# Kernel optimization log

Hardware: AMD Instinct MI355X
Metric: run time of the kernel (lower is better)

Reference implementation:

```python
import jax, jax.numpy as jnp
import numpy as np

D_MODEL = 1024
NHEAD = 8
HEAD_DIM = D_MODEL // NHEAD
D_FF = 4096
EPS_ATTN = 1e-6
EPS_LN = 1e-5


def _layernorm(x, g, b):
    mu = jnp.mean(x, axis=-1, keepdims=True)
    var = jnp.var(x, axis=-1, keepdims=True)
    return (x - mu) * jax.lax.rsqrt(var + EPS_LN) * g + b


def _linear_attention(q, k, v):
    # q,k,v: [N, L, H, D]
    Q = jax.nn.elu(q) + 1.0
    K = jax.nn.elu(k) + 1.0
    v_length = v.shape[1]
    v = v / v_length
    KV = jnp.einsum('nshd,nshv->nhdv', K, v)           # [N,H,D,D]
    Z = 1.0 / (jnp.einsum('nlhd,nhd->nlh', Q, K.sum(axis=1)) + EPS_ATTN)
    out = jnp.einsum('nlhd,nhdv,nlh->nlhv', Q, KV, Z) * v_length
    return out


def setup_inputs() -> dict:
    key = jax.random.key(0)
    ks = jax.random.split(key, 12)
    s = 1.0 / np.sqrt(D_MODEL)
    sf = 1.0 / np.sqrt(D_FF)
    return {
        'x': jax.random.normal(ks[0], (2, 4096, D_MODEL), jnp.float32),
        'wq': jax.random.normal(ks[1], (D_MODEL, D_MODEL), jnp.float32) * s,
        'wk': jax.random.normal(ks[2], (D_MODEL, D_MODEL), jnp.float32) * s,
        'wv': jax.random.normal(ks[3], (D_MODEL, D_MODEL), jnp.float32) * s,
        'w1': jax.random.normal(ks[4], (D_FF, D_MODEL), jnp.float32) * s,
        'b1': jnp.zeros((D_FF,), jnp.float32),
        'w2': jax.random.normal(ks[5], (D_MODEL, D_FF), jnp.float32) * sf,
        'b2': jnp.zeros((D_MODEL,), jnp.float32),
        'g1': jnp.ones((D_MODEL,), jnp.float32),
        'be1': jnp.zeros((D_MODEL,), jnp.float32),
        'g2': jnp.ones((D_MODEL,), jnp.float32),
        'be2': jnp.zeros((D_MODEL,), jnp.float32),
    }


def reference(x, wq, wk, wv, w1, b1, w2, b2, g1, be1, g2, be2):
    N, L, C = x.shape
    # pre-norm self attention
    x2 = _layernorm(x, g1, be1)
    q = (x2 @ wq.T).reshape(N, L, NHEAD, HEAD_DIM)
    k = (x2 @ wk.T).reshape(N, L, NHEAD, HEAD_DIM)
    v = (x2 @ wv.T).reshape(N, L, NHEAD, HEAD_DIM)
    msg = _linear_attention(q, k, v).reshape(N, L, C)
    x = x + msg
    # MLP block
    x2 = _layernorm(x, g2, be2)
    h = jax.nn.gelu(x2 @ w1.T + b1, approximate=False)
    x = x + (h @ w2.T + b2)
    return x
```

## Files before the change

kernel.cpp:

```cpp
#include <hip/hip_runtime.h>
#include <hip/hip_bf16.h>
#include <math.h>

typedef __bf16 bf16x8 __attribute__((ext_vector_type(8)));
typedef __bf16 bf16x4 __attribute__((ext_vector_type(4)));
typedef float f32x4 __attribute__((ext_vector_type(4)));

#define DEVI __device__ __forceinline__

DEVI void gload_lds16(const __bf16* g, __bf16* l) {
    __builtin_amdgcn_global_load_lds(
        (const __attribute__((address_space(1))) unsigned int*)g,
        (__attribute__((address_space(3))) unsigned int*)l, 16, 0, 0);
}

DEVI float fast_erf(float x) {
    const float ax = __builtin_fabsf(x);
    const float t = __builtin_amdgcn_rcpf(__builtin_fmaf(0.3275911f, ax, 1.0f));
    float p = __builtin_fmaf(1.061405429f, t, -1.453152027f);
    p = __builtin_fmaf(p, t, 1.421413741f);
    p = __builtin_fmaf(p, t, -0.284496736f);
    p = __builtin_fmaf(p, t, 0.254829592f);
    const float e = __expf(-ax * ax);
    const float r = __builtin_fmaf(-p * t, e, 1.0f);
    return __builtin_copysignf(r, x);
}

DEVI float gelu_exact(float v) {
    return 0.5f * v * (1.0f + fast_erf(v * 0.70710678118654752f));
}

DEVI int swz128(int row, int col) { return row * 128 + (col ^ ((row & 7) << 3)); }

__global__ void sniff_kernel(const unsigned short* __restrict__ x, int* flags) {
    const int tid = threadIdx.x;
    const unsigned short u = x[tid * 2];
    const int e = (u >> 7) & 0xFF;
    const int zero = (u == 0) ? 1 : 0;
    const int sane = ((e >= 0x71 && e <= 0x8E) || ((u & 0x7FFF) == 0)) ? 1 : 0;
    const unsigned long long mz = __ballot(zero != 0);
    const unsigned long long ms = __ballot(sane != 0);
    __shared__ int wz[4], wsn[4];
    if ((tid & 63) == 0) { wz[tid >> 6] = __popcll(mz); wsn[tid >> 6] = __popcll(ms); }
    __syncthreads();
    if (tid == 0) {
        const int nz = wz[0] + wz[1] + wz[2] + wz[3];
        const int ns = wsn[0] + wsn[1] + wsn[2] + wsn[3];
        flags[0] = (nz >= 192 || ns < 128) ? 1 : 0;
    }
}

DEVI void conv8(const void* src, __bf16* dst, int si, int di, int isf32) {
    if (isf32) {
        const float* s = (const float*)src + si;
        bf16x8 o;
#pragma unroll
        for (int j = 0; j < 8; j++) o[j] = (__bf16)s[j];
        *(bf16x8*)(dst + di) = o;
    } else {
        *(uint4*)(dst + di) = *(const uint4*)((const __bf16*)src + si);
    }
}

__global__ __launch_bounds__(256) void convert_kernel(const void* __restrict__ src,
                                                      __bf16* __restrict__ dst, int n,
                                                      const int* __restrict__ flags) {
    const int i = (blockIdx.x * 256 + threadIdx.x) * 8;
    if (i >= n) return;
    conv8(src, dst, i, i, flags[0]);
}

__global__ __launch_bounds__(256) void convert3_kernel(const void* s0, const void* s1,
                                                       const void* s2, __bf16* __restrict__ dst,
                                                       const int* __restrict__ flags) {
    const int i = (blockIdx.x * 256 + threadIdx.x) * 8;
    const int which = i >> 20;
    const int off = i & 1048575;
    const void* s = (which == 0) ? s0 : ((which == 1) ? s1 : s2);
    conv8(s, dst, off, i, flags[0]);
}

struct Ptr6 { const void* p[6]; };
__global__ __launch_bounds__(256) void convert_small(Ptr6 srcs, __bf16* __restrict__ d0,
                                                     __bf16* __restrict__ d1,
                                                     const int* __restrict__ flags) {
    const int idx = (blockIdx.x * 256 + threadIdx.x) * 8;
    if (idx >= 9216) return;
    const int f = flags[0];
    if (idx < 4096) {
        conv8(srcs.p[0], d0, idx, idx, f);
    } else {
        const int j = idx - 4096;
        conv8(srcs.p[1 + (j >> 10)], d1, j & 1023, j, f);
    }
}

__global__ __launch_bounds__(256) void convert_ln_kernel(
    const void* __restrict__ src, const __bf16* __restrict__ g,
    const __bf16* __restrict__ b, __bf16* __restrict__ cx,
    __bf16* __restrict__ x2, const int* __restrict__ flags) {
    const size_t row = blockIdx.x;
    const int tid = threadIdx.x;
    float v[4];
    if (flags[0]) {
        const float4 f = *((const float4*)((const float*)src + row * 1024) + tid);
        v[0] = f.x; v[1] = f.y; v[2] = f.z; v[3] = f.w;
    } else {
        const bf16x4 f = *((const bf16x4*)((const __bf16*)src + row * 1024) + tid);
#pragma unroll
        for (int i = 0; i < 4; i++) v[i] = (float)f[i];
    }
    bf16x4 o;
#pragma unroll
    for (int i = 0; i < 4; i++) o[i] = (__bf16)v[i];
    *((bf16x4*)(cx + row * 1024) + tid) = o;

    float s = v[0] + v[1] + v[2] + v[3];
    float s2 = v[0] * v[0] + v[1] * v[1] + v[2] * v[2] + v[3] * v[3];
#pragma unroll
    for (int m = 32; m >= 1; m >>= 1) {
        s += __shfl_xor(s, m, 64);
        s2 += __shfl_xor(s2, m, 64);
    }
    __shared__ float rs[4], rs2[4];
    const int wave = tid >> 6, lane = tid & 63;
    if (lane == 0) { rs[wave] = s; rs2[wave] = s2; }
    __syncthreads();
    s = rs[0] + rs[1] + rs[2] + rs[3];
    s2 = rs2[0] + rs2[1] + rs2[2] + rs2[3];
    const float mu = s * (1.0f / 1024.0f);
    const float var = s2 * (1.0f / 1024.0f) - mu * mu;
    const float inv = rsqrtf(var + 1e-5f);
#pragma unroll
    for (int i = 0; i < 4; i++) {
        const int c = tid * 4 + i;
        x2[row * 1024 + c] = (__bf16)((v[i] - mu) * inv * (float)g[c] + (float)b[c]);
    }
}

template <typename T>
__global__ __launch_bounds__(256) void ln_kernel(const T* __restrict__ x,
                                                 const __bf16* __restrict__ g,
                                                 const __bf16* __restrict__ b,
                                                 __bf16* __restrict__ out) {
    const size_t row = blockIdx.x;
    const T* xr = x + row * 1024;
    const int tid = threadIdx.x;
    float v[4];
#pragma unroll
    for (int i = 0; i < 4; i++) v[i] = (float)xr[tid * 4 + i];
    float s = v[0] + v[1] + v[2] + v[3];
    float s2 = v[0] * v[0] + v[1] * v[1] + v[2] * v[2] + v[3] * v[3];
#pragma unroll
    for (int m = 32; m >= 1; m >>= 1) {
        s += __shfl_xor(s, m, 64);
        s2 += __shfl_xor(s2, m, 64);
    }
    __shared__ float rs[4], rs2[4];
    const int wave = tid >> 6, lane = tid & 63;
    if (lane == 0) { rs[wave] = s; rs2[wave] = s2; }
    __syncthreads();
    s = rs[0] + rs[1] + rs[2] + rs[3];
    s2 = rs2[0] + rs2[1] + rs2[2] + rs2[3];
    const float mu = s * (1.0f / 1024.0f);
    const float var = s2 * (1.0f / 1024.0f) - mu * mu;
    const float inv = rsqrtf(var + 1e-5f);
#pragma unroll
    for (int i = 0; i < 4; i++) {
        const int c = tid * 4 + i;
        out[row * 1024 + c] = (__bf16)((v[i] - mu) * inv * (float)g[c] + (float)b[c]);
    }
}

enum { EP_NONE = 0, EP_ELU1 = 1, EP_BIAS_GELU = 2, EP_BIAS_RES = 3, EP_QKV = 4 };

template <int EP, typename OutT>
__global__ __launch_bounds__(256, 4) void gemm_bt(
    const __bf16* __restrict__ A, const __bf16* __restrict__ B,
    const __bf16* __restrict__ bias, const float* resid,
    OutT* C, int M, int N, int K) {
    const int nwg = gridDim.x * gridDim.y;
    int bid = blockIdx.y * gridDim.x + blockIdx.x;
    bid = (bid & 7) * (nwg >> 3) + (bid >> 3);
    const int bm = bid / gridDim.x, bn = bid % gridDim.x;

    const int tid = threadIdx.x;
    const int wave = tid >> 6, lane = tid & 63;
    const int wm = wave & 1, wn = wave >> 1;
    const int lm = lane & 15, lq = lane >> 4;

    __shared__ __align__(16) __bf16 Asmem[2][128 * 32];
    __shared__ __align__(16) __bf16 Bsmem[2][128 * 32];

    f32x4 acc[4][4] = {};

    const __bf16* Abase = A + (size_t)bm * 128 * K;
    const __bf16* Bbase = B + (size_t)bn * 128 * K;

    const int sr = tid >> 2;
    const int sc = (((tid & 3) ^ ((tid >> 3) & 3))) << 3;
    const int wb = wave * 512;

    const __bf16* Ap0 = Abase + (size_t)sr * K + sc;
    const __bf16* Ap1 = Abase + (size_t)(sr + 64) * K + sc;
    const __bf16* Bp0 = Bbase + (size_t)sr * K + sc;
    const __bf16* Bp1 = Bbase + (size_t)(sr + 64) * K + sc;

    const int rg = ((lq ^ ((lm >> 1) & 3))) << 3;

#define STAGE(b, kk)                              \
    do {                                          \
        gload_lds16(Ap0 + (kk), &Asmem[b][wb]);   \
        gload_lds16(Ap1 + (kk), &Asmem[b][2048 + wb]); \
        gload_lds16(Bp0 + (kk), &Bsmem[b][wb]);   \
        gload_lds16(Bp1 + (kk), &Bsmem[b][2048 + wb]); \
    } while (0)

    STAGE(0, 0);
    __syncthreads();
    int cur = 0;
    for (int k0 = 0; k0 < K; k0 += 32) {
        if (k0 + 32 < K) STAGE(cur ^ 1, k0 + 32);
        bf16x8 af[4], bfv[4];
#pragma unroll
        for (int i = 0; i < 4; i++) {
            af[i]  = *(const bf16x8*)&Asmem[cur][(wm * 64 + i * 16 + lm) * 32 + rg];
            bfv[i] = *(const bf16x8*)&Bsmem[cur][(wn * 64 + i * 16 + lm) * 32 + rg];
        }
#pragma unroll
        for (int i = 0; i < 4; i++)
#pragma unroll
            for (int j = 0; j < 4; j++)
                acc[i][j] = __builtin_amdgcn_mfma_f32_16x16x32_bf16(af[i], bfv[j], acc[i][j], 0, 0, 0);
        __syncthreads();
        cur ^= 1;
    }
#undef STAGE

    const int row0 = bm * 128 + wm * 64;
    const int col0 = bn * 128 + wn * 64;
#pragma unroll
    for (int i = 0; i < 4; i++) {
#pragma unroll
        for (int j = 0; j < 4; j++) {
            const int col = col0 + j * 16 + lm;
#pragma unroll
            for (int r = 0; r < 4; r++) {
                const int row = row0 + i * 16 + lq * 4 + r;
                float v = acc[i][j][r];
                if (EP == EP_QKV) {
                    const int which = col >> 10;
                    if (which < 2) v = (v > 0.0f) ? (v + 1.0f) : __expf(v);
                    ((__bf16*)C)[(size_t)which * 8388608 + (size_t)row * 1024 + (col & 1023)] = (__bf16)v;
                    continue;
                }
                if (EP == EP_ELU1) {
                    v = (v > 0.0f) ? (v + 1.0f) : __expf(v);
                } else if (EP == EP_BIAS_GELU) {
                    v += (float)bias[col];
                    v = gelu_exact(v);
                } else if (EP == EP_BIAS_RES) {
                    v += (float)bias[col];
                    v += resid[(size_t)row * N + col];
                }
                C[(size_t)row * N + col] = (OutT)v;
            }
        }
    }
}

__global__ __launch_bounds__(512, 2) void gemm256_gelu(
    const __bf16* __restrict__ A, const __bf16* __restrict__ B,
    const __bf16* __restrict__ bias, __bf16* __restrict__ C,
    int M, int N, int K) {
    const int nwg = gridDim.x * gridDim.y;
    int bid = blockIdx.y * gridDim.x + blockIdx.x;
    bid = (bid & 7) * (nwg >> 3) + (bid >> 3);
    const int bm = bid / gridDim.x, bn = bid % gridDim.x;

    const int tid = threadIdx.x;
    const int wave = tid >> 6, lane = tid & 63;
    const int wm = wave >> 2, wn = wave & 3;
    const int lm = lane & 15, lq = lane >> 4;

    __shared__ __align__(16) __bf16 Asmem[2][256 * 64];
    __shared__ __align__(16) __bf16 Bsmem[2][256 * 64];

    f32x4 acc[8][4] = {};

    const int sr = tid >> 3;
    const int sc = (((tid & 7) ^ ((tid >> 3) & 7))) << 3;
    const int wdst = wave * 512;

    const __bf16* Ap[4];
    const __bf16* Bp[4];
#pragma unroll
    for (int p = 0; p < 4; p++) {
        Ap[p] = A + (size_t)(bm * 256 + p * 64 + sr) * K + sc;
        Bp[p] = B + (size_t)(bn * 256 + p * 64 + sr) * K + sc;
    }

#define STAGE256(b, kk)                                          \
    do {                                                         \
        _Pragma("unroll")                                        \
        for (int p = 0; p < 4; p++) {                            \
            gload_lds16(Ap[p] + (kk), &Asmem[b][p * 4096 + wdst]); \
            gload_lds16(Bp[p] + (kk), &Bsmem[b][p * 4096 + wdst]); \
        }                                                        \
    } while (0)

    STAGE256(0, 0);
    STAGE256(1, 64);
    asm volatile("s_waitcnt vmcnt(8)" ::: "memory");
    __builtin_amdgcn_s_barrier();
    asm volatile("" ::: "memory");

    const int gsw = lm & 7;
    const int nt = K >> 6;
    int cur = 0;
    for (int t = 0; t < nt; ++t) {
#pragma unroll
        for (int ks = 0; ks < 2; ks++) {
            const int rg = ((ks * 4 + lq) ^ gsw) << 3;
            bf16x8 af[8], bv[4];
#pragma unroll
            for (int i = 0; i < 8; i++)
                af[i] = *(const bf16x8*)&Asmem[cur][(wm * 128 + i * 16 + lm) * 64 + rg];
#pragma unroll
            for (int j = 0; j < 4; j++)
                bv[j] = *(const bf16x8*)&Bsmem[cur][(wn * 64 + j * 16 + lm) * 64 + rg];
            __builtin_amdgcn_s_setprio(1);
#pragma unroll
            for (int i = 0; i < 8; i++)
#pragma unroll
                for (int j = 0; j < 4; j++)
                    acc[i][j] = __builtin_amdgcn_mfma_f32_16x16x32_bf16(af[i], bv[j], acc[i][j], 0, 0, 0);
            __builtin_amdgcn_s_setprio(0);
        }
        asm volatile("" ::: "memory");
        __builtin_amdgcn_s_barrier();
        asm volatile("" ::: "memory");
        if (t + 2 < nt) {
            STAGE256(cur, (t + 2) << 6);
            asm volatile("s_waitcnt vmcnt(8)" ::: "memory");
        } else {
            asm volatile("s_waitcnt vmcnt(0)" ::: "memory");
        }
        __builtin_amdgcn_s_barrier();
        asm volatile("" ::: "memory");
        cur ^= 1;
    }
#undef STAGE256

    const int row0 = bm * 256 + wm * 128;
    const int col0 = bn * 256 + wn * 64;
#pragma unroll
    for (int i = 0; i < 8; i++) {
#pragma unroll
        for (int j = 0; j < 4; j++) {
            const int col = col0 + j * 16 + lm;
            const float bcol = (float)bias[col];
#pragma unroll
            for (int r = 0; r < 4; r++) {
                const int row = row0 + i * 16 + lq * 4 + r;
                C[(size_t)row * N + col] = (__bf16)gelu_exact(acc[i][j][r] + bcol);
            }
        }
    }
}

__global__ __launch_bounds__(256, 2) void gemm_bt_k64(
    const __bf16* __restrict__ A, const __bf16* __restrict__ B,
    const __bf16* __restrict__ bias, const float* resid,
    float* C, int M, int N, int K) {
    const int nwg = gridDim.x * gridDim.y;
    int bid = blockIdx.y * gridDim.x + blockIdx.x;
    bid = (bid & 7) * (nwg >> 3) + (bid >> 3);
    const int bm = bid / gridDim.x, bn = bid % gridDim.x;

    const int tid = threadIdx.x;
    const int wave = tid >> 6, lane = tid & 63;
    const int wm = wave & 1, wn = wave >> 1;
    const int lm = lane & 15, lq = lane >> 4;

    __shared__ __align__(16) __bf16 Asmem[2][128 * 64];
    __shared__ __align__(16) __bf16 Bsmem[2][128 * 64];

    f32x4 acc[4][4] = {};

    const __bf16* Abase = A + (size_t)bm * 128 * K;
    const __bf16* Bbase = B + (size_t)bn * 128 * K;

    const int sr = tid >> 3;
    const int sc = (((tid & 7) ^ ((tid >> 3) & 7))) << 3;
    const int wb = wave * 512;

    const __bf16* Ap[4];
    const __bf16* Bp[4];
#pragma unroll
    for (int p = 0; p < 4; p++) {
        Ap[p] = Abase + (size_t)(p * 32 + sr) * K + sc;
        Bp[p] = Bbase + (size_t)(p * 32 + sr) * K + sc;
    }

#define STAGE64(b, kk)                                        \
    do {                                                      \
        _Pragma("unroll")                                     \
        for (int p = 0; p < 4; p++) {                         \
            gload_lds16(Ap[p] + (kk), &Asmem[b][p * 2048 + wb]); \
            gload_lds16(Bp[p] + (kk), &Bsmem[b][p * 2048 + wb]); \
        }                                                     \
    } while (0)

    STAGE64(0, 0);
    __syncthreads();
    int cur = 0;
    for (int k0 = 0; k0 < K; k0 += 64) {
        if (k0 + 64 < K) STAGE64(cur ^ 1, k0 + 64);
        bf16x8 af[2][4], bfv[2][4];
#pragma unroll
        for (int h = 0; h < 2; h++) {
            const int rg = ((h * 4 + lq) ^ (lm & 7)) << 3;
#pragma unroll
            for (int i = 0; i < 4; i++) {
                af[h][i]  = *(const bf16x8*)&Asmem[cur][(wm * 64 + i * 16 + lm) * 64 + rg];
                bfv[h][i] = *(const bf16x8*)&Bsmem[cur][(wn * 64 + i * 16 + lm) * 64 + rg];
            }
        }
#pragma unroll
        for (int h = 0; h < 2; h++)
#pragma unroll
            for (int i = 0; i < 4; i++)
#pragma unroll
                for (int j = 0; j < 4; j++)
                    acc[i][j] = __builtin_amdgcn_mfma_f32_16x16x32_bf16(af[h][i], bfv[h][j], acc[i][j], 0, 0, 0);
        __syncthreads();
        cur ^= 1;
    }
#undef STAGE64

    const int row0 = bm * 128 + wm * 64;
    const int col0 = bn * 128 + wn * 64;
#pragma unroll
    for (int i = 0; i < 4; i++) {
#pragma unroll
        for (int j = 0; j < 4; j++) {
            const int col = col0 + j * 16 + lm;
            const float bcol = (float)bias[col];
#pragma unroll
            for (int r = 0; r < 4; r++) {
                const int row = row0 + i * 16 + lq * 4 + r;
                float v = acc[i][j][r] + bcol;
                v += resid[(size_t)row * N + col];
                C[(size_t)row * N + col] = v;
            }
        }
    }
}

__global__ __launch_bounds__(256) void kv_kernel(const __bf16* __restrict__ Kf,
                                                 const __bf16* __restrict__ Vf,
                                                 float* __restrict__ pkv,
                                                 float* __restrict__ pks) {
    const int nh = blockIdx.x, sc = blockIdx.y, vh = blockIdx.z;
    const int n = nh >> 3, h = nh & 7;
    const int tid = threadIdx.x;
    const int tv = tid & 15, td = tid >> 4;
    __shared__ __align__(16) __bf16 Kt[32 * 128];
    __shared__ __align__(16) __bf16 Vt[32 * 64];
    float acc[8][4] = {};
    float ks[8] = {};
    const size_t rowbase = (size_t)n * 4096 + (size_t)sc * 256;
    for (int s0 = 0; s0 < 256; s0 += 32) {
#pragma unroll
        for (int rep = 0; rep < 2; rep++) {
            const int s = tid + rep * 256;
            const int r = s >> 4, cs = (s & 15) * 8;
            const size_t gidx = (rowbase + s0 + r) * 1024 + h * 128 + cs;
            *(bf16x8*)&Kt[r * 128 + cs] = *(const bf16x8*)&Kf[gidx];
        }
        {
            const int r = tid >> 3, cs = (tid & 7) * 8;
            const size_t gidx = (rowbase + s0 + r) * 1024 + h * 128 + vh * 64 + cs;
            *(bf16x8*)&Vt[r * 64 + cs] = *(const bf16x8*)&Vf[gidx];
        }
        __syncthreads();
#pragma unroll 4
        for (int s = 0; s < 32; s++) {
            const bf16x8 k8 = *(const bf16x8*)&Kt[s * 128 + td * 8];
            const bf16x4 v4 = *(const bf16x4*)&Vt[s * 64 + tv * 4];
            float kk[8], vv[4];
#pragma unroll
            for (int i = 0; i < 8; i++) kk[i] = (float)k8[i];
#pragma unroll
            for (int j = 0; j < 4; j++) vv[j] = (float)v4[j];
#pragma unroll
            for (int i = 0; i < 8; i++) {
                ks[i] += kk[i];
#pragma unroll
                for (int j = 0; j < 4; j++) acc[i][j] += kk[i] * vv[j];
            }
        }
        __syncthreads();
    }
    float* dst = pkv + ((size_t)sc * 16 + nh) * 16384;
#pragma unroll
    for (int j = 0; j < 4; j++)
#pragma unroll
        for (int i = 0; i < 8; i++)
            dst[(vh * 64 + tv * 4 + j) * 128 + td * 8 + i] = acc[i][j];
    if (vh == 0 && tv == 0) {
        float* ds2 = pks + ((size_t)sc * 16 + nh) * 128;
#pragma unroll
        for (int i = 0; i < 8; i++) ds2[td * 8 + i] = ks[i];
    }
}

__global__ __launch_bounds__(256) void kv_reduce(const float* __restrict__ pkv,
                                                 const float* __restrict__ pks,
                                                 __bf16* __restrict__ kvbT,
                                                 float* __restrict__ ksf) {
    const int idx = blockIdx.x * 256 + threadIdx.x;
    float s = 0.0f;
#pragma unroll
    for (int c = 0; c < 16; c++) s += pkv[(size_t)c * 262144 + idx];
    kvbT[idx] = (__bf16)s;
    if (idx < 2048) {
        float t = 0.0f;
#pragma unroll
        for (int c = 0; c < 16; c++) t += pks[c * 2048 + idx];
        ksf[idx] = t;
    }
}

__global__ __launch_bounds__(256) void z_kernel(const __bf16* __restrict__ Qf,
                                                const float* __restrict__ ksf,
                                                float* __restrict__ zbuf) {
    const int idx = blockIdx.x * 256 + threadIdx.x;
    const int h = idx & 7;
    const size_t row = (size_t)(idx >> 3);
    const __bf16* q = Qf + row * 1024 + h * 128;
    const float* ks = ksf + ((size_t)((row >> 12) * 8 + h)) * 128;
    float s = 0.0f;
    for (int d = 0; d < 128; d += 8) {
        const bf16x8 q8 = *(const bf16x8*)&q[d];
#pragma unroll
        for (int j = 0; j < 8; j++) s += (float)q8[j] * ks[d + j];
    }
    zbuf[idx] = 1.0f / (s + 1e-6f);
}

__global__ __launch_bounds__(256, 3) void attn_out_kernel(
    const __bf16* __restrict__ x, const __bf16* __restrict__ Qf,
    const __bf16* __restrict__ kvbT, const float* __restrict__ zbuf,
    float* __restrict__ xmid) {
    const int nh = blockIdx.x, lc = blockIdx.y;
    const int n = nh >> 3, h = nh & 7;
    const int tid = threadIdx.x;
    const int wv = tid >> 6, lane = tid & 63;
    const int lm = lane & 15, lq = lane >> 4;
    __shared__ __align__(16) __bf16 KVs[128 * 128];
    __shared__ __align__(16) __bf16 Qs[64 * 128];
    __shared__ float Zs[64];
    const __bf16* kv = kvbT + (size_t)nh * 16384;
#pragma unroll
    for (int rep = 0; rep < 8; rep++) {
        const int i = tid + rep * 256;
        const int r = i >> 4, c8 = (i & 15) * 8;
        *(bf16x8*)&KVs[swz128(r, c8)] = *(const bf16x8*)&kv[i * 8];
    }
    const size_t gr0 = (size_t)n * 4096 + (size_t)lc * 64;
#pragma unroll
    for (int rep = 0; rep < 4; rep++) {
        const int s = tid + rep * 256;
        const int r = s >> 4, cs = (s & 15) * 8;
        *(bf16x8*)&Qs[swz128(r, cs)] =
            *(const bf16x8*)&Qf[(gr0 + r) * 1024 + h * 128 + cs];
    }
    if (tid < 64) Zs[tid] = zbuf[(gr0 + tid) * 8 + h];
    __syncthreads();

    const int xmask = (lm & 7) << 3;
    f32x4 acc[4][2] = {};
#pragma unroll
    for (int k0 = 0; k0 < 128; k0 += 32) {
        const int kk = (k0 + lq * 8) ^ xmask;
        bf16x8 af[4], bv[2];
#pragma unroll
        for (int i = 0; i < 4; i++)
            af[i] = *(const bf16x8*)&Qs[(i * 16 + lm) * 128 + kk];
#pragma unroll
        for (int j = 0; j < 2; j++)
            bv[j] = *(const bf16x8*)&KVs[(wv * 32 + j * 16 + lm) * 128 + kk];
#pragma unroll
        for (int i = 0; i < 4; i++)
#pragma unroll
            for (int j = 0; j < 2; j++)
                acc[i][j] = __builtin_amdgcn_mfma_f32_16x16x32_bf16(af[i], bv[j], acc[i][j], 0, 0, 0);
    }
#pragma unroll
    for (int i = 0; i < 4; i++) {
#pragma unroll
        for (int j = 0; j < 2; j++) {
            const int col = wv * 32 + j * 16 + lm;
#pragma unroll
            for (int r = 0; r < 4; r++) {
                const int lr = i * 16 + lq * 4 + r;
                const size_t gi = (gr0 + lr) * 1024 + h * 128 + col;
                xmid[gi] = (float)x[gi] + acc[i][j][r] * Zs[lr];
            }
        }
    }
}

extern "C" void kernel_launch(void* const* d_in, const int* in_sizes, int n_in,
                              void* d_out, int out_size, void* d_ws, size_t ws_size,
                              hipStream_t stream) {
    float* out = (float*)d_out;
    char* ws = (char*)d_ws;

    const int nx = 8388608, nw = 1048576, nw1 = 4194304, nb1 = 4096, ng = 1024;
    size_t off = 0;
    __bf16* cx   = (__bf16*)(ws + off); off += (size_t)nx * 2;
    __bf16* cwq  = (__bf16*)(ws + off); off += (size_t)nw * 2;
    __bf16* cwk  = (__bf16*)(ws + off); off += (size_t)nw * 2;
    __bf16* cwv  = (__bf16*)(ws + off); off += (size_t)nw * 2;
    __bf16* cw1  = (__bf16*)(ws + off); off += (size_t)nw1 * 2;
    __bf16* cb1  = (__bf16*)(ws + off); off += (size_t)nb1 * 2;
    __bf16* cw2  = (__bf16*)(ws + off); off += (size_t)nw1 * 2;
    __bf16* cb2  = (__bf16*)(ws + off); off += (size_t)ng * 2;
    __bf16* cg1  = (__bf16*)(ws + off); off += (size_t)ng * 2;
    __bf16* cbe1 = (__bf16*)(ws + off); off += (size_t)ng * 2;
    __bf16* cg2  = (__bf16*)(ws + off); off += (size_t)ng * 2;
    __bf16* cbe2 = (__bf16*)(ws + off); off += (size_t)ng * 2;
    int* flags = (int*)(ws + off); off += 64;
    (void)cwk; (void)cwv; (void)cg1; (void)cbe1; (void)cg2; (void)cbe2;

    char* PB = ws + off;
    __bf16* x2   = (__bf16*)(PB);
    __bf16* Qf   = (__bf16*)(PB + 16777216);
    __bf16* Kf   = (__bf16*)(PB + 33554432);
    __bf16* Vf   = (__bf16*)(PB + 50331648);
    float*  pkv  = (float*)(PB + 67108864);
    float*  pks  = (float*)(PB + 83886080);
    float*  ksf  = (float*)(PB + 84017152);
    float*  zbuf = (float*)(PB + 84025344);
    __bf16* kvbT = (__bf16*)(PB + 84287488);
    __bf16* hbuf = (__bf16*)(PB + 16777216);
    float*  xmid = out;

    sniff_kernel<<<1, 256, 0, stream>>>((const unsigned short*)d_in[0], flags);
    convert3_kernel<<<3 * nw / 2048, 256, 0, stream>>>(d_in[1], d_in[2], d_in[3], cwq, flags);
    convert_kernel<<<nw1 / 2048, 256, 0, stream>>>(d_in[4], cw1, nw1, flags);
    convert_kernel<<<nw1 / 2048, 256, 0, stream>>>(d_in[6], cw2, nw1, flags);
    Ptr6 sp;
    sp.p[0] = d_in[5];  sp.p[1] = d_in[7];  sp.p[2] = d_in[8];
    sp.p[3] = d_in[9];  sp.p[4] = d_in[10]; sp.p[5] = d_in[11];
    convert_small<<<5, 256, 0, stream>>>(sp, cb1, cb2, flags);

    convert_ln_kernel<<<8192, 256, 0, stream>>>(d_in[0], cg1, cbe1, cx, x2, flags);
    gemm_bt<EP_QKV, __bf16><<<dim3(3072 / 128, 8192 / 128), 256, 0, stream>>>(
        x2, cwq, nullptr, nullptr, Qf, 8192, 3072, 1024);
    kv_kernel<<<dim3(16, 16, 2), 256, 0, stream>>>(Kf, Vf, pkv, pks);
    kv_reduce<<<1024, 256, 0, stream>>>(pkv, pks, kvbT, ksf);
    z_kernel<<<256, 256, 0, stream>>>(Qf, ksf, zbuf);
    attn_out_kernel<<<dim3(16, 64), 256, 0, stream>>>(cx, Qf, kvbT, zbuf, xmid);
    ln_kernel<float><<<8192, 256, 0, stream>>>(xmid, cg2, cbe2, x2);
    gemm256_gelu<<<dim3(4096 / 256, 8192 / 256), 512, 0, stream>>>(
        x2, cw1, cb1, hbuf, 8192, 4096, 1024);
    gemm_bt_k64<<<dim3(1024 / 128, 8192 / 128), 256, 0, stream>>>(
        hbuf, cw2, cb2, xmid, out, 8192, 1024, 4096);
}
```

Baseline: 467.1 us.

## Split GELU GEMM k-loop into barrier-separated phases interleaving LDS reads, MFMA and prefetch

Restructures the 256x256 GELU GEMM main loop into four phases per k-tile. Each phase issues a quarter of the next tile's global-to-LDS loads, reads half the A fragments, and runs 16 MFMAs, with a workgroup barrier between phases, in a ping-pong schedule. Prefetch depth drops from two tiles ahead to one, and launch bounds change from 2 to 1 workgroups per CU, freeing registers. The aim is to overlap memory traffic with MFMA work inside a single large workgroup. The extra barriers and lower occupancy could expose latency instead of hiding it.

```diff
diff --git a/kernel.cpp b/kernel.cpp
--- a/kernel.cpp
+++ b/kernel.cpp
@@ -269,7 +269,7 @@
     }
 }
 
-__global__ __launch_bounds__(512, 2) void gemm256_gelu(
+__global__ __launch_bounds__(512, 1) void gemm256_gelu(
     const __bf16* __restrict__ A, const __bf16* __restrict__ B,
     const __bf16* __restrict__ bias, __bf16* __restrict__ C,
     int M, int N, int K) {
@@ -300,57 +300,92 @@
         Bp[p] = B + (size_t)(bn * 256 + p * 64 + sr) * K + sc;
     }
 
-#define STAGE256(b, kk)                                          \
-    do {                                                         \
-        _Pragma("unroll")                                        \
-        for (int p = 0; p < 4; p++) {                            \
-            gload_lds16(Ap[p] + (kk), &Asmem[b][p * 4096 + wdst]); \
-            gload_lds16(Bp[p] + (kk), &Bsmem[b][p * 4096 + wdst]); \
-        }                                                        \
+#define STAGE2(b, kk, w)                                                     \
+    do {                                                                     \
+        if ((w) == 0) {                                                      \
+            gload_lds16(Ap[0] + (kk), &Asmem[b][0 * 4096 + wdst]);           \
+            gload_lds16(Ap[1] + (kk), &Asmem[b][1 * 4096 + wdst]);           \
+        } else if ((w) == 1) {                                               \
+            gload_lds16(Ap[2] + (kk), &Asmem[b][2 * 4096 + wdst]);           \
+            gload_lds16(Ap[3] + (kk), &Asmem[b][3 * 4096 + wdst]);           \
+        } else if ((w) == 2) {                                               \
+            gload_lds16(Bp[0] + (kk), &Bsmem[b][0 * 4096 + wdst]);           \
+            gload_lds16(Bp[1] + (kk), &Bsmem[b][1 * 4096 + wdst]);           \
+        } else {                                                             \
+            gload_lds16(Bp[2] + (kk), &Bsmem[b][2 * 4096 + wdst]);           \
+            gload_lds16(Bp[3] + (kk), &Bsmem[b][3 * 4096 + wdst]);           \
+        }                                                                    \
     } while (0)
 
-    STAGE256(0, 0);
-    STAGE256(1, 64);
-    asm volatile("s_waitcnt vmcnt(8)" ::: "memory");
-    __builtin_amdgcn_s_barrier();
-    asm volatile("" ::: "memory");
+#define PH_DSREAD_AF(ihalf, rg)                                              \
+    _Pragma("unroll")                                                        \
+    for (int i = 0; i < 4; i++)                                              \
+        af[i] = *(const bf16x8*)&Asmem[cur][(wm * 128 + ((ihalf) * 4 + i) * 16 + lm) * 64 + (rg)];
+#define PH_DSREAD_BV(rg)                                                     \
+    _Pragma("unroll")                                                        \
+    for (int j = 0; j < 4; j++)                                              \
+        bv[j] = *(const bf16x8*)&Bsmem[cur][(wn * 64 + j * 16 + lm) * 64 + (rg)];
+#define PH_MFMA(ihalf)                                                       \
+    __builtin_amdgcn_s_setprio(1);                                           \
+    _Pragma("unroll")                                                        \
+    for (int i = 0; i < 4; i++)                                              \
+        _Pragma("unroll")                                                    \
+        for (int j = 0; j < 4; j++)                                          \
+            acc[(ihalf) * 4 + i][j] = __builtin_amdgcn_mfma_f32_16x16x32_bf16( \
+                af[i], bv[j], acc[(ihalf) * 4 + i][j], 0, 0, 0);             \
+    __builtin_amdgcn_s_setprio(0);
+#define PH_BAR()                                                             \
+    asm volatile("" ::: "memory");                                           \
+    __builtin_amdgcn_s_barrier();                                            \
+    asm volatile("" ::: "memory")
+
+    STAGE2(0, 0, 0);
+    STAGE2(0, 0, 1);
+    STAGE2(0, 0, 2);
+    STAGE2(0, 0, 3);
+    asm volatile("s_waitcnt vmcnt(0)" ::: "memory");
+    PH_BAR();
 
     const int gsw = lm & 7;
     const int nt = K >> 6;
     int cur = 0;
     for (int t = 0; t < nt; ++t) {
-#pragma unroll
-        for (int ks = 0; ks < 2; ks++) {
-            const int rg = ((ks * 4 + lq) ^ gsw) << 3;
-            bf16x8 af[8], bv[4];
-#pragma unroll
-            for (int i = 0; i < 8; i++)
-                af[i] = *(const bf16x8*)&Asmem[cur][(wm * 128 + i * 16 + lm) * 64 + rg];
-#pragma unroll
-            for (int j = 0; j < 4; j++)
-                bv[j] = *(const bf16x8*)&Bsmem[cur][(wn * 64 + j * 16 + lm) * 64 + rg];
-            __builtin_amdgcn_s_setprio(1);
-#pragma unroll
-            for (int i = 0; i < 8; i++)
-#pragma unroll
-                for (int j = 0; j < 4; j++)
-                    acc[i][j] = __builtin_amdgcn_mfma_f32_16x16x32_bf16(af[i], bv[j], acc[i][j], 0, 0, 0);
-            __builtin_amdgcn_s_setprio(0);
-        }
-        asm volatile("" ::: "memory");
-        __builtin_amdgcn_s_barrier();
-        asm volatile("" ::: "memory");
-        if (t + 2 < nt) {
-            STAGE256(cur, (t + 2) << 6);
-            asm volatile("s_waitcnt vmcnt(8)" ::: "memory");
-        } else {
-            asm volatile("s_waitcnt vmcnt(0)" ::: "memory");
-        }
-        __builtin_amdgcn_s_barrier();
-        asm volatile("" ::: "memory");
+        const int nb = cur ^ 1;
+        const bool pf = (t + 1 < nt);
+        const int nk = (t + 1) << 6;
+        const int rg0 = (lq ^ gsw) << 3;
+        const int rg1 = ((4 + lq) ^ gsw) << 3;
+        bf16x8 af[4], bv[4];
+        PH_DSREAD_BV(rg0);
+        PH_DSREAD_AF(0, rg0);
+        if (pf) STAGE2(nb, nk, 0);
+        PH_BAR();
+        PH_MFMA(0);
+        PH_BAR();
+        PH_DSREAD_AF(1, rg0);
+        if (pf) STAGE2(nb, nk, 1);
+        PH_BAR();
+        PH_MFMA(1);
+        PH_BAR();
+        PH_DSREAD_BV(rg1);
+        PH_DSREAD_AF(0, rg1);
+        if (pf) STAGE2(nb, nk, 2);
+        PH_BAR();
+        PH_MFMA(0);
+        PH_BAR();
+        PH_DSREAD_AF(1, rg1);
+        if (pf) STAGE2(nb, nk, 3);
+        PH_BAR();
+        PH_MFMA(1);
+        if (pf) asm volatile("s_waitcnt vmcnt(0)" ::: "memory");
+        PH_BAR();
         cur ^= 1;
     }
-#undef STAGE256
+#undef STAGE2
+#undef PH_DSREAD_AF
+#undef PH_DSREAD_BV
+#undef PH_MFMA
+#undef PH_BAR
 
     const int row0 = bm * 256 + wm * 128;
     const int col0 = bn * 256 + wn * 64;
```

New measurement: 456.3 us (median of 3 runs). 1.02x faster.
